# Kernel optimization log

Measured on AMD Instinct MI355X. Metric: run time of the kernel, lower is better.

Reference implementation:

```python
import jax, jax.numpy as jnp
import numpy as np

V, H, O = 50257, 512, 4
B, T = 64, 512


def setup_inputs() -> dict:
    key = jax.random.key(0)
    ks = jax.random.split(key, 8)
    s = 1.0 / np.sqrt(H)
    return {
        "input_ids": jax.random.randint(ks[0], (B, T), 0, V),
        "labels": jax.random.randint(ks[1], (B,), 0, O),
        "emb": jax.random.normal(ks[2], (V, H), dtype=jnp.float32) * s,
        "W_in": jax.random.normal(ks[3], (H, H), dtype=jnp.float32) * s,   # linear_input.weight [out,in], no bias
        "W_h": jax.random.normal(ks[4], (H, H), dtype=jnp.float32) * s,    # linear_hidden.weight
        "b_h": jax.random.normal(ks[5], (H,), dtype=jnp.float32) * s,      # linear_hidden.bias
        "W_out": jax.random.normal(ks[6], (O, H), dtype=jnp.float32) * s,  # linear_output.weight
        "b_out": jax.random.normal(ks[7], (O,), dtype=jnp.float32) * s,
    }


def reference(input_ids, labels, emb, W_in, W_h, b_h, W_out, b_out):
    # Embed all tokens up front: [B, T, H] -> scan over time [T, B, H]
    x = emb[input_ids]
    xs = jnp.swapaxes(x, 0, 1)
    h0 = jnp.zeros((input_ids.shape[0], W_h.shape[0]), dtype=emb.dtype)

    def step(h, x_t):
        # Elman cell: relu(x W_in^T + h W_h^T + b_h)
        h_new = jax.nn.relu(x_t @ W_in.T + h @ W_h.T + b_h)
        return h_new, None

    h_T, _ = jax.lax.scan(step, h0, xs)
    # NOTE: original applies Softmax BEFORE CrossEntropyLoss (faithful bug reproduction)
    logits = jax.nn.softmax(h_T @ W_out.T + b_out, axis=1)
    logp = jax.nn.log_softmax(logits, axis=1)
    loss = -jnp.take_along_axis(logp, labels[:, None], axis=1).mean()
    return loss, logits
```

## Files before the change

### kernel.cpp

```cpp
#include <hip/hip_runtime.h>


typedef _Float16 f16;
typedef _Float16 half2_t __attribute__((ext_vector_type(2)));
typedef _Float16 half8_t __attribute__((ext_vector_type(8)));
typedef float f32x4 __attribute__((ext_vector_type(4)));

#define HDIM 512
#define BATCH 64
#define TSTEPS 512
#define OUTC 4

__device__ __forceinline__ float dot2f(unsigned int h, unsigned int w, float acc) {
#if __has_builtin(__builtin_amdgcn_fdot2)
  return __builtin_amdgcn_fdot2(__builtin_bit_cast(half2_t, h),
                                __builtin_bit_cast(half2_t, w), acc, false);
#else
  half2_t a = __builtin_bit_cast(half2_t, h);
  half2_t b = __builtin_bit_cast(half2_t, w);
  return acc + (float)a.x * (float)b.x + (float)a.y * (float)b.y;
#endif
}

__global__ void convert_w(const float* __restrict__ Win, const float* __restrict__ Wh,
                          f16* __restrict__ wif, f16* __restrict__ whf) {
  int i = blockIdx.x * 256 + threadIdx.x;
  if (i < HDIM * HDIM) {
    wif[i] = (f16)Win[i];
    whf[i] = (f16)Wh[i];
  }
}

__global__ __launch_bounds__(256) void gemm_pre(const int* __restrict__ ids,
                                                const float* __restrict__ emb,
                                                const f16* __restrict__ wif,
                                                const float* __restrict__ bh,
                                                f16* __restrict__ preh) {
  __shared__ __align__(16) f16 Al[64][40];
  __shared__ __align__(16) f16 Bl[64][40];

  const int tid = threadIdx.x;
  const int rb = blockIdx.x;
  const int nb = blockIdx.y;
  const int w = tid >> 6;
  const int l = tid & 63;

  f32x4 acc[4] = {};

  const int srow = tid >> 2;
  const int quad = tid & 3;

  for (int k0 = 0; k0 < HDIM; k0 += 32) {
    {
      int rg = rb * 64 + srow;
      int id = ids[(rg & 63) * TSTEPS + (rg >> 6)];
      const float4* s = (const float4*)(emb + id * HDIM + k0 + quad * 8);
      float4 a0 = s[0], a1 = s[1];
      half8_t v;
      v[0] = (f16)a0.x; v[1] = (f16)a0.y; v[2] = (f16)a0.z; v[3] = (f16)a0.w;
      v[4] = (f16)a1.x; v[5] = (f16)a1.y; v[6] = (f16)a1.z; v[7] = (f16)a1.w;
      *(half8_t*)&Al[srow][quad * 8] = v;
    }
    {
      const uint4* s = (const uint4*)(wif + (nb * 64 + srow) * HDIM + k0 + quad * 8);
      *(uint4*)&Bl[srow][quad * 8] = s[0];
    }
    __syncthreads();

    half8_t af = *(const half8_t*)&Al[w * 16 + (l & 15)][(l >> 4) * 8];
#pragma unroll
    for (int nt = 0; nt < 4; ++nt) {
      half8_t bf = *(const half8_t*)&Bl[nt * 16 + (l & 15)][(l >> 4) * 8];
      acc[nt] = __builtin_amdgcn_mfma_f32_16x16x32_f16(af, bf, acc[nt], 0, 0, 0);
    }
    __syncthreads();
  }

#pragma unroll
  for (int nt = 0; nt < 4; ++nt) {
#pragma unroll
    for (int i = 0; i < 4; ++i) {
      int r = rb * 64 + w * 16 + (l >> 4) * 4 + i;
      int c = nb * 64 + nt * 16 + (l & 15);
      preh[r * HDIM + c] = (f16)(acc[nt][i] + bh[c]);
    }
  }
}

__global__ __launch_bounds__(512, 2) void rnn_steps(const f16* __restrict__ preh,
                                                    const f16* __restrict__ whf,
                                                    float* __restrict__ hT) {
  __shared__ __align__(16) uint4 wlds[HDIM * 16];
  __shared__ __align__(16) unsigned int hb[2][HDIM / 2];

  const int j = threadIdx.x;
  const int b = blockIdx.x;

  for (int q = 0; q < 16; ++q) {
    int idx = q * 512 + j;
    int row = idx >> 4, c = idx & 15;
    uint4 v = *(const uint4*)(whf + row * HDIM + 384 + c * 8);
    wlds[row * 16 + (c ^ (row & 15))] = v;
  }
  uint4 wr[48];
  {
    const uint4* wrow = (const uint4*)(whf + j * HDIM);
#pragma unroll
    for (int c = 0; c < 48; ++c) wr[c] = wrow[c];
  }
  if (j < HDIM / 2) hb[0][j] = 0u;
  __syncthreads();

  float pre_cur = (float)preh[b * HDIM + j];
  for (int t = 0; t < TSTEPS; ++t) {
    float pre_next = 0.f;
    if (t < TSTEPS - 1) pre_next = (float)preh[((t + 1) * BATCH + b) * HDIM + j];

    const uint4* hp = (const uint4*)hb[t & 1];
    float acc = pre_cur;
#pragma unroll
    for (int c = 0; c < 48; ++c) {
      uint4 h4 = hp[c];
      acc = dot2f(h4.x, wr[c].x, acc);
      acc = dot2f(h4.y, wr[c].y, acc);
      acc = dot2f(h4.z, wr[c].z, acc);
      acc = dot2f(h4.w, wr[c].w, acc);
    }
    const uint4* wl = &wlds[j * 16];
    const int sw = j & 15;
#pragma unroll
    for (int c = 0; c < 16; ++c) {
      uint4 h4 = hp[48 + c];
      uint4 w4 = wl[c ^ sw];
      acc = dot2f(h4.x, w4.x, acc);
      acc = dot2f(h4.y, w4.y, acc);
      acc = dot2f(h4.z, w4.z, acc);
      acc = dot2f(h4.w, w4.w, acc);
    }
    acc = fmaxf(acc, 0.f);
    ((f16*)hb[(t + 1) & 1])[j] = (f16)acc;
    if (t == TSTEPS - 1) hT[b * HDIM + j] = acc;
    pre_cur = pre_next;
    __syncthreads();
  }
}

__global__ void tail_kernel(const float* __restrict__ hT, const float* __restrict__ Wout,
                            const float* __restrict__ bout, const int* __restrict__ labels,
                            float* __restrict__ out) {
  __shared__ float lred[BATCH];
  const int b = threadIdx.x;
  const float4* hr = (const float4*)(hT + b * HDIM);
  const float4* w0 = (const float4*)(Wout + 0 * HDIM);
  const float4* w1 = (const float4*)(Wout + 1 * HDIM);
  const float4* w2 = (const float4*)(Wout + 2 * HDIM);
  const float4* w3 = (const float4*)(Wout + 3 * HDIM);
  float z0 = bout[0], z1 = bout[1], z2 = bout[2], z3 = bout[3];
#pragma unroll 4
  for (int k = 0; k < HDIM / 4; ++k) {
    float4 h = hr[k];
    float4 a = w0[k], c = w1[k], d = w2[k], e = w3[k];
    z0 += h.x * a.x + h.y * a.y + h.z * a.z + h.w * a.w;
    z1 += h.x * c.x + h.y * c.y + h.z * c.z + h.w * c.w;
    z2 += h.x * d.x + h.y * d.y + h.z * d.z + h.w * d.w;
    z3 += h.x * e.x + h.y * e.y + h.z * e.z + h.w * e.w;
  }
  float m = fmaxf(fmaxf(z0, z1), fmaxf(z2, z3));
  float e0 = __expf(z0 - m), e1 = __expf(z1 - m), e2 = __expf(z2 - m), e3 = __expf(z3 - m);
  float se = e0 + e1 + e2 + e3;
  float p0 = e0 / se, p1 = e1 / se, p2 = e2 / se, p3 = e3 / se;
  float m2 = fmaxf(fmaxf(p0, p1), fmaxf(p2, p3));
  float s2 = __expf(p0 - m2) + __expf(p1 - m2) + __expf(p2 - m2) + __expf(p3 - m2);
  float lse = m2 + __logf(s2);
  int lab = labels[b];
  float pl = (lab == 0) ? p0 : (lab == 1) ? p1 : (lab == 2) ? p2 : p3;
  lred[b] = pl - lse;
  out[1 + b * 4 + 0] = p0;
  out[1 + b * 4 + 1] = p1;
  out[1 + b * 4 + 2] = p2;
  out[1 + b * 4 + 3] = p3;
  __syncthreads();
  if (b == 0) {
    float s = 0.f;
#pragma unroll
    for (int i = 0; i < BATCH; ++i) s += lred[i];
    out[0] = -s / (float)BATCH;
  }
}

extern "C" void kernel_launch(void* const* d_in, const int* in_sizes, int n_in,
                              void* d_out, int out_size, void* d_ws, size_t ws_size,
                              hipStream_t stream) {
  const int* ids = (const int*)d_in[0];
  const int* labels = (const int*)d_in[1];
  const float* emb = (const float*)d_in[2];
  const float* Win = (const float*)d_in[3];
  const float* Wh = (const float*)d_in[4];
  const float* bh = (const float*)d_in[5];
  const float* Wout = (const float*)d_in[6];
  const float* bout = (const float*)d_in[7];
  float* out = (float*)d_out;

  char* ws = (char*)d_ws;
  f16* whf = (f16*)ws;
  f16* wif = (f16*)(ws + (512 << 10));
  f16* preh = (f16*)(ws + (1 << 20));
  float* hT = (float*)(ws + (1 << 20) + (32 << 20));

  convert_w<<<dim3(1024), dim3(256), 0, stream>>>(Win, Wh, wif, whf);
  gemm_pre<<<dim3(512, 8), dim3(256), 0, stream>>>(ids, emb, wif, bh, preh);
  rnn_steps<<<dim3(64), dim3(512), 0, stream>>>(preh, whf, hT);
  tail_kernel<<<dim3(1), dim3(64), 0, stream>>>(hT, Wout, bout, labels, out);
}
```

Before: 1.161 ms.

## Split embedding gather into separate f16 pass and pin RNN weights in registers

Adds a kernel that gathers embedding rows and converts them to f16 once, so the pre-activation GEMM reads a contiguous f16 matrix. Previously the gather and fp32 read were repeated across the eight column blocks. The RNN step kernel now keeps its weights as scalar u32 registers, with asm volatile barriers so the compiler does not spill or reload them. The trade-off is an extra 32MB f16 buffer write and read, plus higher register pressure.

Result: slower. 1.187 ms (+2.3%).

```diff
diff --git a/kernel.cpp b/kernel.cpp
--- a/kernel.cpp
+++ b/kernel.cpp
@@ -5,6 +5,7 @@
 typedef _Float16 half2_t __attribute__((ext_vector_type(2)));
 typedef _Float16 half8_t __attribute__((ext_vector_type(8)));
 typedef float f32x4 __attribute__((ext_vector_type(4)));
+typedef unsigned int u32x4 __attribute__((ext_vector_type(4)));
 
 #define HDIM 512
 #define BATCH 64
@@ -31,8 +32,23 @@
   }
 }
 
-__global__ __launch_bounds__(256) void gemm_pre(const int* __restrict__ ids,
-                                                const float* __restrict__ emb,
+__global__ __launch_bounds__(256) void embed_f16(const int* __restrict__ ids,
+                                                 const float* __restrict__ emb,
+                                                 f16* __restrict__ xh) {
+  int gid = blockIdx.x * 256 + threadIdx.x;
+  int r = gid >> 7;
+  int lane = gid & 127;
+  int id = ids[(r & 63) * TSTEPS + (r >> 6)];
+  float4 a = *(const float4*)(emb + id * HDIM + lane * 4);
+  half2_t lo, hi;
+  lo.x = (f16)a.x; lo.y = (f16)a.y;
+  hi.x = (f16)a.z; hi.y = (f16)a.w;
+  half2_t* dst = (half2_t*)(xh + r * HDIM + lane * 4);
+  dst[0] = lo;
+  dst[1] = hi;
+}
+
+__global__ __launch_bounds__(256) void gemm_pre(const f16* __restrict__ xh,
                                                 const f16* __restrict__ wif,
                                                 const float* __restrict__ bh,
                                                 f16* __restrict__ preh) {
@@ -51,20 +67,10 @@
   const int quad = tid & 3;
 
   for (int k0 = 0; k0 < HDIM; k0 += 32) {
-    {
-      int rg = rb * 64 + srow;
-      int id = ids[(rg & 63) * TSTEPS + (rg >> 6)];
-      const float4* s = (const float4*)(emb + id * HDIM + k0 + quad * 8);
-      float4 a0 = s[0], a1 = s[1];
-      half8_t v;
-      v[0] = (f16)a0.x; v[1] = (f16)a0.y; v[2] = (f16)a0.z; v[3] = (f16)a0.w;
-      v[4] = (f16)a1.x; v[5] = (f16)a1.y; v[6] = (f16)a1.z; v[7] = (f16)a1.w;
-      *(half8_t*)&Al[srow][quad * 8] = v;
-    }
-    {
-      const uint4* s = (const uint4*)(wif + (nb * 64 + srow) * HDIM + k0 + quad * 8);
-      *(uint4*)&Bl[srow][quad * 8] = s[0];
-    }
+    *(u32x4*)&Al[srow][quad * 8] =
+        *(const u32x4*)(xh + (rb * 64 + srow) * HDIM + k0 + quad * 8);
+    *(u32x4*)&Bl[srow][quad * 8] =
+        *(const u32x4*)(wif + (nb * 64 + srow) * HDIM + k0 + quad * 8);
     __syncthreads();
 
     half8_t af = *(const half8_t*)&Al[w * 16 + (l & 15)][(l >> 4) * 8];
@@ -90,7 +96,7 @@
 __global__ __launch_bounds__(512, 2) void rnn_steps(const f16* __restrict__ preh,
                                                     const f16* __restrict__ whf,
                                                     float* __restrict__ hT) {
-  __shared__ __align__(16) uint4 wlds[HDIM * 16];
+  __shared__ __align__(16) u32x4 wlds[HDIM * 16];
   __shared__ __align__(16) unsigned int hb[2][HDIM / 2];
 
   const int j = threadIdx.x;
@@ -99,15 +105,26 @@
   for (int q = 0; q < 16; ++q) {
     int idx = q * 512 + j;
     int row = idx >> 4, c = idx & 15;
-    uint4 v = *(const uint4*)(whf + row * HDIM + 384 + c * 8);
+    u32x4 v = *(const u32x4*)(whf + row * HDIM + 384 + c * 8);
     wlds[row * 16 + (c ^ (row & 15))] = v;
   }
-  uint4 wr[48];
+
+  unsigned int wr[192];
   {
-    const uint4* wrow = (const uint4*)(whf + j * HDIM);
-#pragma unroll
-    for (int c = 0; c < 48; ++c) wr[c] = wrow[c];
-  }
+    const u32x4* wrow = (const u32x4*)(whf + j * HDIM);
+#pragma unroll
+    for (int c = 0; c < 48; ++c) {
+      u32x4 v = wrow[c];
+      wr[4 * c + 0] = v[0];
+      wr[4 * c + 1] = v[1];
+      wr[4 * c + 2] = v[2];
+      wr[4 * c + 3] = v[3];
+    }
+  }
+#pragma unroll
+  for (int c = 0; c < 192; c += 4)
+    asm volatile("" : "+v"(wr[c]), "+v"(wr[c + 1]), "+v"(wr[c + 2]), "+v"(wr[c + 3]));
+
   if (j < HDIM / 2) hb[0][j] = 0u;
   __syncthreads();
 
@@ -116,26 +133,26 @@
     float pre_next = 0.f;
     if (t < TSTEPS - 1) pre_next = (float)preh[((t + 1) * BATCH + b) * HDIM + j];
 
-    const uint4* hp = (const uint4*)hb[t & 1];
+    const u32x4* hp = (const u32x4*)hb[t & 1];
     float acc = pre_cur;
 #pragma unroll
     for (int c = 0; c < 48; ++c) {
-      uint4 h4 = hp[c];
-      acc = dot2f(h4.x, wr[c].x, acc);
-      acc = dot2f(h4.y, wr[c].y, acc);
-      acc = dot2f(h4.z, wr[c].z, acc);
-      acc = dot2f(h4.w, wr[c].w, acc);
-    }
-    const uint4* wl = &wlds[j * 16];
+      u32x4 h4 = hp[c];
+      acc = dot2f(h4[0], wr[4 * c + 0], acc);
+      acc = dot2f(h4[1], wr[4 * c + 1], acc);
+      acc = dot2f(h4[2], wr[4 * c + 2], acc);
+      acc = dot2f(h4[3], wr[4 * c + 3], acc);
+    }
+    const u32x4* wl = &wlds[j * 16];
     const int sw = j & 15;
 #pragma unroll
     for (int c = 0; c < 16; ++c) {
-      uint4 h4 = hp[48 + c];
-      uint4 w4 = wl[c ^ sw];
-      acc = dot2f(h4.x, w4.x, acc);
-      acc = dot2f(h4.y, w4.y, acc);
-      acc = dot2f(h4.z, w4.z, acc);
-      acc = dot2f(h4.w, w4.w, acc);
+      u32x4 h4 = hp[48 + c];
+      u32x4 w4 = wl[c ^ sw];
+      acc = dot2f(h4[0], w4[0], acc);
+      acc = dot2f(h4[1], w4[1], acc);
+      acc = dot2f(h4[2], w4[2], acc);
+      acc = dot2f(h4[3], w4[3], acc);
     }
     acc = fmaxf(acc, 0.f);
     ((f16*)hb[(t + 1) & 1])[j] = (f16)acc;
@@ -205,10 +222,12 @@
   f16* whf = (f16*)ws;
   f16* wif = (f16*)(ws + (512 << 10));
   f16* preh = (f16*)(ws + (1 << 20));
-  float* hT = (float*)(ws + (1 << 20) + (32 << 20));
+  f16* xh = (f16*)(ws + (1 << 20) + (32 << 20));
+  float* hT = (float*)(ws + (1 << 20) + (64 << 20));
 
   convert_w<<<dim3(1024), dim3(256), 0, stream>>>(Win, Wh, wif, whf);
-  gemm_pre<<<dim3(512, 8), dim3(256), 0, stream>>>(ids, emb, wif, bh, preh);
+  embed_f16<<<dim3((BATCH * TSTEPS * 128) / 256), dim3(256), 0, stream>>>(ids, emb, xh);
+  gemm_pre<<<dim3(512, 8), dim3(256), 0, stream>>>(xh, wif, bh, preh);
   rnn_steps<<<dim3(64), dim3(512), 0, stream>>>(preh, whf, hT);
   tail_kernel<<<dim3(1), dim3(64), 0, stream>>>(hT, Wout, bout, labels, out);
 }
```
